# Kernel optimization log

Hardware: AMD Instinct MI355X
Metric: run time of the kernel (lower is better)

The kernel has to match this reference:

```python
import jax, jax.numpy as jnp
import numpy as np

NEG_SLOPE = 0.2


def _gat_layer(x, src, dst, W, att_src, att_dst, bias, concat):
    # x: [N, F_in]; W: [F_in, H*C]; att_*: [H, C]; bias: [H*C] or [C]
    N = x.shape[0]
    H, C = att_src.shape
    h = (x @ W).reshape(N, H, C)                      # [N, H, C]
    a_src = jnp.einsum('nhc,hc->nh', h, att_src)      # [N, H]
    a_dst = jnp.einsum('nhc,hc->nh', h, att_dst)      # [N, H]
    e = jax.nn.leaky_relu(a_src[src] + a_dst[dst], NEG_SLOPE)  # [E, H]
    # segment softmax over incoming edges of each destination node
    m = jax.ops.segment_max(e, dst, num_segments=N)   # [N, H]
    ex = jnp.exp(e - m[dst])
    s = jax.ops.segment_sum(ex, dst, num_segments=N)  # [N, H]
    alpha = ex / s[dst]                               # [E, H]
    out = jax.ops.segment_sum(h[src] * alpha[:, :, None], dst, num_segments=N)  # [N,H,C]
    out = out.reshape(N, H * C) if concat else out.mean(axis=1)
    return out + bias


def setup_inputs() -> dict:
    key = jax.random.key(0)
    ks = jax.random.split(key, 16)
    N, E, F = 50000, 1600000, 128
    HC1, H1 = 32, 4
    HC2, H2 = 32, 2
    NC, H3 = 2, 1     # layer3: 64 -> 2, 1 head, concat=False
    g = lambda k, shape, scale: jax.random.normal(k, shape, dtype=jnp.float32) * scale
    return {
        'x': g(ks[0], (N, F), 1.0),
        'edge_index': jax.random.randint(ks[1], (2, E), 0, N, dtype=jnp.int32),
        'W1': g(ks[2], (F, H1 * HC1), 0.1),
        'as1': g(ks[3], (H1, HC1), 0.1),
        'ad1': g(ks[4], (H1, HC1), 0.1),
        'b1': jnp.zeros((H1 * HC1,), jnp.float32),
        'W2': g(ks[5], (H1 * HC1, H2 * HC2), 0.1),
        'as2': g(ks[6], (H2, HC2), 0.1),
        'ad2': g(ks[7], (H2, HC2), 0.1),
        'b2': jnp.zeros((H2 * HC2,), jnp.float32),
        'W3': g(ks[8], (H2 * HC2, H3 * NC), 0.1),
        'as3': g(ks[9], (H3, NC), 0.1),
        'ad3': g(ks[10], (H3, NC), 0.1),
        'b3': jnp.zeros((NC,), jnp.float32),
    }


def reference(x, edge_index, W1, as1, ad1, b1, W2, as2, ad2, b2, W3, as3, ad3, b3):
    N = x.shape[0]
    # PyG GATConv adds self-loops by default
    loops = jnp.arange(N, dtype=edge_index.dtype)
    ei = jnp.concatenate([edge_index, jnp.stack([loops, loops])], axis=1)
    src, dst = ei[0], ei[1]
    h = _gat_layer(x, src, dst, W1, as1, ad1, b1, concat=True)
    h = jax.nn.elu(h)
    h = _gat_layer(h, src, dst, W2, as2, ad2, b2, concat=True)
    h = jax.nn.elu(h)
    h = _gat_layer(h, src, dst, W3, as3, ad3, b3, concat=False)
    return jax.nn.log_softmax(h, axis=1)
```

## Files before the change

### kernel.cpp

```cpp
#include <hip/hip_runtime.h>
#include <hip/hip_bf16.h>

#define NEG_SLOPE 0.2f
#define ARENA 10240

typedef __attribute__((ext_vector_type(8))) short short8v;
typedef __attribute__((ext_vector_type(4))) float f32x4;

__device__ __forceinline__ float bf_lo(uint32_t u) { return __uint_as_float(u << 16); }
__device__ __forceinline__ float bf_hi(uint32_t u) { return __uint_as_float(u & 0xffff0000u); }
__device__ __forceinline__ unsigned short f2bf(float f) {
    uint32_t u = __float_as_uint(f);
    u += 0x7fffu + ((u >> 16) & 1u);
    return (unsigned short)(u >> 16);
}
__device__ __forceinline__ float bf2f(unsigned short h) {
    return __uint_as_float((uint32_t)h << 16);
}

__device__ __forceinline__ int k_of(int l, int j) {
    return (l >> 4) * 4 + (j & 3) + 16 * (j >> 2);
}

template<int FIN, int FOUT>
__global__ void packW_kernel(const float* __restrict__ W, unsigned short* __restrict__ Wp) {
    constexpr int NT = FOUT / 16, KC = FIN / 32;
    int tid = blockIdx.x * blockDim.x + threadIdx.x;
    if (tid >= KC * NT * 64) return;
    int l  = tid & 63;
    int nt = (tid >> 6) % NT;
    int q  = tid / (64 * NT);
    int n  = nt * 16 + (l & 15);
    #pragma unroll
    for (int j = 0; j < 8; ++j) {
        int k = q * 32 + k_of(l, j);
        float v = W[k * FOUT + n];
        unsigned short h = f2bf(v);
        unsigned short lo = f2bf(v - bf2f(h));
        Wp[(((size_t)0 * KC + q) * NT + nt) * 512 + l * 8 + j] = h;
        Wp[(((size_t)1 * KC + q) * NT + nt) * 512 + l * 8 + j] = lo;
    }
}

template<int FIN, int FOUT, int H>
__global__ __launch_bounds__(256) void gemm_mfma_kernel(const float* __restrict__ X,
        const unsigned short* __restrict__ Wp, unsigned short* __restrict__ Hout,
        float* __restrict__ a_src, float* __restrict__ a_dst,
        const float* __restrict__ att_s, const float* __restrict__ att_d, int N) {
    constexpr int NT = FOUT / 16, KC = FIN / 32;
    __shared__ float sX[4][16 * FIN];
    int wv = threadIdx.x >> 6, l = threadIdx.x & 63;
    int mtile = blockIdx.x * 4 + wv;
    if (mtile * 16 >= N) return;
    const float* xsrc = X + (size_t)mtile * 16 * FIN;
    float* lds = sX[wv];
    #pragma unroll
    for (int i = 0; i < (16 * FIN) / 256; ++i) {
        int fi = (i * 64 + l) * 4;
        *(float4*)&lds[fi] = *(const float4*)&xsrc[fi];
    }
    __threadfence_block();

    int koff[8];
    #pragma unroll
    for (int j = 0; j < 8; ++j) koff[j] = k_of(l, j);
    int arow = (l & 15) * FIN;

    f32x4 acc[NT];
    #pragma unroll
    for (int nt = 0; nt < NT; ++nt) acc[nt] = f32x4{0.f, 0.f, 0.f, 0.f};

    const short8v* wp8 = (const short8v*)Wp;
    for (int q = 0; q < KC; ++q) {
        short8v ahi, alo;
        #pragma unroll
        for (int j = 0; j < 8; ++j) {
            float v = lds[arow + q * 32 + koff[j]];
            unsigned short h = f2bf(v);
            ahi[j] = (short)h;
            alo[j] = (short)f2bf(v - bf2f(h));
        }
        #pragma unroll
        for (int nt = 0; nt < NT; ++nt) {
            short8v bhi = wp8[((0 * KC + q) * NT + nt) * 64 + l];
            short8v blo = wp8[((1 * KC + q) * NT + nt) * 64 + l];
            acc[nt] = __builtin_amdgcn_mfma_f32_16x16x32_bf16(ahi, bhi, acc[nt], 0, 0, 0);
            acc[nt] = __builtin_amdgcn_mfma_f32_16x16x32_bf16(alo, bhi, acc[nt], 0, 0, 0);
            acc[nt] = __builtin_amdgcn_mfma_f32_16x16x32_bf16(ahi, blo, acc[nt], 0, 0, 0);
        }
    }

    float as_v[NT], ad_v[NT];
    #pragma unroll
    for (int nt = 0; nt < NT; ++nt) {
        as_v[nt] = att_s[nt * 16 + (l & 15)];
        ad_v[nt] = att_d[nt * 16 + (l & 15)];
    }
    float ps[4][H], pd[4][H];
    #pragma unroll
    for (int r = 0; r < 4; ++r)
        #pragma unroll
        for (int h = 0; h < H; ++h) { ps[r][h] = 0.f; pd[r][h] = 0.f; }
    #pragma unroll
    for (int nt = 0; nt < NT; ++nt)
        #pragma unroll
        for (int r = 0; r < 4; ++r) {
            ps[r][nt >> 1] += acc[nt][r] * as_v[nt];
            pd[r][nt >> 1] += acc[nt][r] * ad_v[nt];
        }
    constexpr int V = 4 * H;
    float* sc = lds;
    int g = l >> 4, l16 = l & 15;
    int base = g * 16 * V + l16 * V;
    __threadfence_block();
    #pragma unroll
    for (int r = 0; r < 4; ++r)
        #pragma unroll
        for (int h = 0; h < H; ++h) {
            sc[base + r * H + h]        = ps[r][h];
            sc[1024 + base + r * H + h] = pd[r][h];
        }
    __threadfence_block();
    if (l16 < V) {
        float S = 0.f, D = 0.f;
        #pragma unroll
        for (int x = 0; x < 16; ++x) {
            S += sc[g * 16 * V + x * V + l16];
            D += sc[1024 + g * 16 * V + x * V + l16];
        }
        int r = l16 / H, h = l16 % H;
        int row = mtile * 16 + g * 4 + r;
        a_src[row * H + h] = S;
        a_dst[row * H + h] = D;
    }

    int row0 = mtile * 16 + (l >> 4) * 4;
    int col  = l & 15;
    #pragma unroll
    for (int nt = 0; nt < NT; ++nt)
        #pragma unroll
        for (int r = 0; r < 4; ++r)
            Hout[(size_t)(row0 + r) * FOUT + nt * 16 + col] = f2bf(acc[nt][r]);
}

__global__ void arena_init_kernel(int* __restrict__ bcur) {
    bcur[threadIdx.x] = threadIdx.x * ARENA;
}

__global__ __launch_bounds__(256) void bkt_scatter_kernel(const int* __restrict__ src,
        const int* __restrict__ dst, int* __restrict__ bcur,
        uint32_t* __restrict__ packed, int E) {
    __shared__ int lh[256], lbase[256], lcur[256];
    int tid = threadIdx.x;
    lh[tid] = 0; lcur[tid] = 0;
    __syncthreads();
    int chunk = (E + gridDim.x - 1) / gridDim.x;
    int e0 = blockIdx.x * chunk;
    int e1 = min(E, e0 + chunk);
    for (int e = e0 + tid; e < e1; e += 256)
        atomicAdd(&lh[dst[e] >> 8], 1);
    __syncthreads();
    if (lh[tid]) lbase[tid] = atomicAdd(&bcur[tid], lh[tid]);
    __syncthreads();
    for (int e = e0 + tid; e < e1; e += 256) {
        int d = dst[e];
        int b = d >> 8;
        int pos = lbase[b] + atomicAdd(&lcur[b], 1);
        packed[pos] = ((uint32_t)(d & 255) << 16) | (uint32_t)src[e];
    }
}

__global__ __launch_bounds__(256) void bkt_sort_kernel(const uint32_t* __restrict__ packed,
        const int* __restrict__ bcur, int* __restrict__ row_ptr, int* __restrict__ degA,
        unsigned short* __restrict__ colw, int N) {
    __shared__ int lh[256], lexcl[256], lcur[256];
    __shared__ int ws4[4];
    int tid = threadIdx.x, lane = tid & 63, wid = tid >> 6;
    int B = blockIdx.x;
    int seg0 = B * ARENA, seg1 = bcur[B];
    lh[tid] = 0; lcur[tid] = 0;
    __syncthreads();
    for (int i = seg0 + tid; i < seg1; i += 256)
        atomicAdd(&lh[packed[i] >> 16], 1);
    __syncthreads();
    int v = lh[tid];
    int x = v;
    #pragma unroll
    for (int off = 1; off < 64; off <<= 1) {
        int t = __shfl_up(x, off);
        if (lane >= off) x += t;
    }
    if (lane == 63) ws4[wid] = x;
    __syncthreads();
    int add = 0;
    #pragma unroll
    for (int w = 0; w < 4; ++w) if (w < wid) add += ws4[w];
    int excl = add + x - v;
    lexcl[tid] = excl;
    int d = B * 256 + tid;
    if (d < N) { row_ptr[d] = seg0 + excl; degA[d] = v; }
    __syncthreads();
    for (int i = seg0 + tid; i < seg1; i += 256) {
        uint32_t p = packed[i];
        int bin = p >> 16;
        int pos = seg0 + lexcl[bin] + atomicAdd(&lcur[bin], 1);
        colw[pos] = (unsigned short)(p & 0xFFFF);
    }
}

template<int H, int C, bool ELU, bool FUSE3>
__global__ __launch_bounds__(256) void agg_fused_kernel(
        const unsigned short* __restrict__ Hb, const float* __restrict__ a_src,
        const float* __restrict__ a_dst, const int* __restrict__ row_ptr,
        const int* __restrict__ degA, const unsigned short* __restrict__ colw,
        const float* __restrict__ bias, float* __restrict__ out,
        const float* __restrict__ W3, const float* __restrict__ as3,
        const float* __restrict__ ad3, float* __restrict__ h3x4, int N) {
    constexpr int HC  = H * C;
    constexpr int LPW = HC / 8;
    constexpr int EPI = 64 / LPW;
    constexpr int SHIFT = (HC == 128) ? 8 : 7;
    static_assert(HC == 128 || HC == 64, "layout");
    __shared__ float sP[4][64 * H];
    __shared__ int   sS[4][64];
    int wv   = threadIdx.x >> 6;
    int lane = threadIdx.x & 63;
    int n = (int)(blockIdx.x * 4 + wv);
    if (n >= N) return;
    int start = row_ptr[n];
    int deg   = degA[n];

    float adv[H], cc[H], sp[H];
    #pragma unroll
    for (int h = 0; h < H; ++h) {
        adv[h] = a_dst[n * H + h];
        cc[h]  = fmaxf(adv[h], 0.f);
        sp[h]  = 0.f;
    }

    int sub = lane / LPW, pl = lane % LPW;
    int elem0 = pl * 8;
    int hh = elem0 / C;
    float a[8];
    #pragma unroll
    for (int j = 0; j < 8; ++j) a[j] = 0.f;

    for (int base = 0; base <= deg; base += 64) {
        int cnt = min(64, deg + 1 - base);
        int idx = base + lane;
        if (idx <= deg) {
            int srcn = (idx < deg) ? (int)colw[start + idx] : n;
            sS[wv][lane] = srcn;
            float av[H];
            if constexpr (H == 4) {
                float4 t = *(const float4*)&a_src[srcn * 4];
                av[0] = t.x; av[1] = t.y; av[2] = t.z; av[3] = t.w;
            } else {
                float2 t = *(const float2*)&a_src[srcn * 2];
                av[0] = t.x; av[1] = t.y;
            }
            #pragma unroll
            for (int h = 0; h < H; ++h) {
                float e = av[h] + adv[h];
                e = (e >= 0.f) ? e : NEG_SLOPE * e;
                float p = __expf(e - cc[h]);
                sp[h] += p;
                sP[wv][lane * H + h] = p;
            }
        }
        __threadfence_block();
        #pragma unroll 4
        for (int k = 0; k < cnt; k += EPI) {
            int eidx = k + sub;
            int eclm = min(eidx, cnt - 1);
            float w  = sP[wv][eclm * H + hh];
            int srcn = sS[wv][eclm];
            if (eidx >= cnt) w = 0.f;
            const char* pb = (const char*)Hb + (((size_t)srcn) << SHIFT) + elem0 * 2;
            uint4 pv = *(const uint4*)pb;
            a[0] = fmaf(w, bf_lo(pv.x), a[0]);
            a[1] = fmaf(w, bf_hi(pv.x), a[1]);
            a[2] = fmaf(w, bf_lo(pv.y), a[2]);
            a[3] = fmaf(w, bf_hi(pv.y), a[3]);
            a[4] = fmaf(w, bf_lo(pv.z), a[4]);
            a[5] = fmaf(w, bf_hi(pv.z), a[5]);
            a[6] = fmaf(w, bf_lo(pv.w), a[6]);
            a[7] = fmaf(w, bf_hi(pv.w), a[7]);
        }
        __threadfence_block();
    }

    #pragma unroll
    for (int off = 32; off; off >>= 1) {
        #pragma unroll
        for (int h = 0; h < H; ++h) sp[h] += __shfl_xor(sp[h], off);
    }
    #pragma unroll
    for (int off = 32; off >= LPW; off >>= 1) {
        #pragma unroll
        for (int j = 0; j < 8; ++j) a[j] += __shfl_xor(a[j], off);
    }
    float inv = 1.f / sp[hh];
    float v[8];
    float4 b40 = *(const float4*)&bias[elem0];
    float4 b41 = *(const float4*)&bias[elem0 + 4];
    v[0] = a[0] * inv + b40.x; v[1] = a[1] * inv + b40.y;
    v[2] = a[2] * inv + b40.z; v[3] = a[3] * inv + b40.w;
    v[4] = a[4] * inv + b41.x; v[5] = a[5] * inv + b41.y;
    v[6] = a[6] * inv + b41.z; v[7] = a[7] * inv + b41.w;
    if (ELU) {
        #pragma unroll
        for (int j = 0; j < 8; ++j) v[j] = (v[j] > 0.f) ? v[j] : __expf(v[j]) - 1.f;
    }
    if constexpr (!FUSE3) {
        if (sub == 0) {
            *(float4*)&out[(size_t)n * HC + elem0]     = make_float4(v[0], v[1], v[2], v[3]);
            *(float4*)&out[(size_t)n * HC + elem0 + 4] = make_float4(v[4], v[5], v[6], v[7]);
        }
    } else {
        float p0 = 0.f, p1 = 0.f;
        #pragma unroll
        for (int j = 0; j < 8; ++j) {
            p0 += v[j] * W3[(elem0 + j) * 2];
            p1 += v[j] * W3[(elem0 + j) * 2 + 1];
        }
        #pragma unroll
        for (int off = 4; off; off >>= 1) {
            p0 += __shfl_xor(p0, off);
            p1 += __shfl_xor(p1, off);
        }
        if (lane == 0) {
            float as = p0 * as3[0] + p1 * as3[1];
            float ad = p0 * ad3[0] + p1 * ad3[1];
            *(float4*)&h3x4[(size_t)n * 4] = make_float4(p0, p1, as, ad);
        }
    }
}

__global__ __launch_bounds__(256) void agg3_kernel(
        const float* __restrict__ h3x4, const int* __restrict__ row_ptr,
        const int* __restrict__ degA, const unsigned short* __restrict__ colw,
        const float* __restrict__ bias, float* __restrict__ out, int N) {
    int wave = (int)((blockIdx.x * blockDim.x + threadIdx.x) >> 6);
    int lane = threadIdx.x & 63;
    if (wave >= N) return;
    int n = wave;
    int start = row_ptr[n];
    int deg   = degA[n];
    float adv = h3x4[(size_t)n * 4 + 3];
    float c   = fmaxf(adv, 0.f);
    float s = 0.f, acc0 = 0.f, acc1 = 0.f;
    for (int i = lane; i <= deg; i += 64) {
        int srcn = (i < deg) ? (int)colw[start + i] : n;
        float4 g = *(const float4*)&h3x4[(size_t)srcn * 4];
        float e = g.z + adv;
        e = (e >= 0.f) ? e : NEG_SLOPE * e;
        float p = __expf(e - c);
        s += p;
        acc0 = fmaf(p, g.x, acc0);
        acc1 = fmaf(p, g.y, acc1);
    }
    #pragma unroll
    for (int off = 32; off; off >>= 1) {
        s    += __shfl_xor(s, off);
        acc0 += __shfl_xor(acc0, off);
        acc1 += __shfl_xor(acc1, off);
    }
    if (lane == 0) {
        float v0 = acc0 / s + bias[0];
        float v1 = acc1 / s + bias[1];
        float mx = fmaxf(v0, v1);
        float lse = mx + logf(__expf(v0 - mx) + __expf(v1 - mx));
        out[n * 2 + 0] = v0 - lse;
        out[n * 2 + 1] = v1 - lse;
    }
}

extern "C" void kernel_launch(void* const* d_in, const int* in_sizes, int n_in,
                              void* d_out, int out_size, void* d_ws, size_t ws_size,
                              hipStream_t stream) {
    const float* x   = (const float*)d_in[0];
    const int*   ei  = (const int*)d_in[1];
    const float* W1  = (const float*)d_in[2];
    const float* as1 = (const float*)d_in[3];
    const float* ad1 = (const float*)d_in[4];
    const float* b1  = (const float*)d_in[5];
    const float* W2  = (const float*)d_in[6];
    const float* as2 = (const float*)d_in[7];
    const float* ad2 = (const float*)d_in[8];
    const float* b2  = (const float*)d_in[9];
    const float* W3  = (const float*)d_in[10];
    const float* as3 = (const float*)d_in[11];
    const float* ad3 = (const float*)d_in[12];
    const float* b3  = (const float*)d_in[13];
    int N = in_sizes[0] / 128;
    int E = in_sizes[1] / 2;
    const int* src = ei;
    const int* dst = ei + E;
    int NB = (N + 255) / 256;

    char* ws = (char*)d_ws;
    size_t off = 0;
    auto alloc = [&](size_t bytes) -> void* {
        void* p = ws + off;
        off = (off + bytes + 255) & ~(size_t)255;
        return p;
    };
    int*            bcur    = (int*)alloc(256 * 4);
    int*            row_ptr = (int*)alloc((size_t)N * 4);
    int*            degA    = (int*)alloc((size_t)N * 4);
    uint32_t*       packed  = (uint32_t*)alloc((size_t)NB * ARENA * 4);
    unsigned short* colw    = (unsigned short*)alloc((size_t)NB * ARENA * 2);
    unsigned short* hb      = (unsigned short*)alloc((size_t)N * 128 * 2);
    float*          obuf    = (float*)alloc((size_t)N * 128 * 4);
    float*          h3x4    = (float*)alloc((size_t)N * 4 * 4);
    float*          asrc    = (float*)alloc((size_t)N * 4 * 4);
    float*          adst    = (float*)alloc((size_t)N * 4 * 4);
    unsigned short* Wp1     = (unsigned short*)alloc((size_t)2 * 4 * 8 * 512 * 2);
    unsigned short* Wp2     = (unsigned short*)alloc((size_t)2 * 4 * 4 * 512 * 2);

    packW_kernel<128, 128><<<8, 256, 0, stream>>>(W1, Wp1);
    packW_kernel<128, 64><<<4, 256, 0, stream>>>(W2, Wp2);

    arena_init_kernel<<<1, 256, 0, stream>>>(bcur);
    bkt_scatter_kernel<<<256, 256, 0, stream>>>(src, dst, bcur, packed, E);
    bkt_sort_kernel<<<NB, 256, 0, stream>>>(packed, bcur, row_ptr, degA, colw, N);

    int gmblocks = ((N + 15) / 16 + 3) / 4;

    gemm_mfma_kernel<128, 128, 4><<<gmblocks, 256, 0, stream>>>(x, Wp1, hb, asrc, adst, as1, ad1, N);
    agg_fused_kernel<4, 32, true, false><<<(N + 3) / 4, 256, 0, stream>>>(
        hb, asrc, adst, row_ptr, degA, colw, b1, obuf, nullptr, nullptr, nullptr, nullptr, N);

    gemm_mfma_kernel<128, 64, 2><<<gmblocks, 256, 0, stream>>>(obuf, Wp2, hb, asrc, adst, as2, ad2, N);
    agg_fused_kernel<2, 32, true, true><<<(N + 3) / 4, 256, 0, stream>>>(
        hb, asrc, adst, row_ptr, degA, colw, b2, nullptr, W3, as3, ad3, h3x4, N);

    agg3_kernel<<<(N + 3) / 4, 256, 0, stream>>>(h3x4, row_ptr, degA, colw, b3, (float*)d_out, N);
}
```

Baseline: 203.2 us.

## Store layer-1 output as bf16 and deepen gather pipelining in aggregation

Result: slower. 209.1 us (+2.9%).

```diff
diff --git a/kernel.cpp b/kernel.cpp
--- a/kernel.cpp
+++ b/kernel.cpp
@@ -90,6 +90,8 @@
         }
     }
 
+    constexpr int V = 4 * H;
+    constexpr int PLOFF = 64 * V;
     float as_v[NT], ad_v[NT];
     #pragma unroll
     for (int nt = 0; nt < NT; ++nt) {
@@ -108,7 +110,6 @@
             ps[r][nt >> 1] += acc[nt][r] * as_v[nt];
             pd[r][nt >> 1] += acc[nt][r] * ad_v[nt];
         }
-    constexpr int V = 4 * H;
     float* sc = lds;
     int g = l >> 4, l16 = l & 15;
     int base = g * 16 * V + l16 * V;
@@ -117,8 +118,8 @@
     for (int r = 0; r < 4; ++r)
         #pragma unroll
         for (int h = 0; h < H; ++h) {
-            sc[base + r * H + h]        = ps[r][h];
-            sc[1024 + base + r * H + h] = pd[r][h];
+            sc[base + r * H + h]         = ps[r][h];
+            sc[PLOFF + base + r * H + h] = pd[r][h];
         }
     __threadfence_block();
     if (l16 < V) {
@@ -126,7 +127,105 @@
         #pragma unroll
         for (int x = 0; x < 16; ++x) {
             S += sc[g * 16 * V + x * V + l16];
-            D += sc[1024 + g * 16 * V + x * V + l16];
+            D += sc[PLOFF + g * 16 * V + x * V + l16];
+        }
+        int r = l16 / H, h = l16 % H;
+        int row = mtile * 16 + g * 4 + r;
+        a_src[row * H + h] = S;
+        a_dst[row * H + h] = D;
+    }
+
+    int row0 = mtile * 16 + (l >> 4) * 4;
+    int col  = l & 15;
+    #pragma unroll
+    for (int nt = 0; nt < NT; ++nt)
+        #pragma unroll
+        for (int r = 0; r < 4; ++r)
+            Hout[(size_t)(row0 + r) * FOUT + nt * 16 + col] = f2bf(acc[nt][r]);
+}
+
+template<int FIN, int FOUT, int H>
+__global__ __launch_bounds__(256) void gemm_mfma_bf16_kernel(const unsigned short* __restrict__ X,
+        const unsigned short* __restrict__ Wp, unsigned short* __restrict__ Hout,
+        float* __restrict__ a_src, float* __restrict__ a_dst,
+        const float* __restrict__ att_s, const float* __restrict__ att_d, int N) {
+    constexpr int NT = FOUT / 16, KC = FIN / 32;
+    constexpr int V = 4 * H;
+    constexpr int PLOFF = 64 * V;
+    __shared__ float sX[4][(16 * FIN) / 2 > 2 * PLOFF ? (16 * FIN) / 2 : 2 * PLOFF];
+    int wv = threadIdx.x >> 6, l = threadIdx.x & 63;
+    int mtile = blockIdx.x * 4 + wv;
+    if (mtile * 16 >= N) return;
+    const unsigned short* xsrc = X + (size_t)mtile * 16 * FIN;
+    float* lds = sX[wv];
+    unsigned short* ldsu = (unsigned short*)lds;
+    #pragma unroll
+    for (int i = 0; i < (16 * FIN) / 512; ++i) {
+        int fi = (i * 64 + l) * 8;
+        *(uint4*)&ldsu[fi] = *(const uint4*)&xsrc[fi];
+    }
+    __threadfence_block();
+
+    int koff[8];
+    #pragma unroll
+    for (int j = 0; j < 8; ++j) koff[j] = k_of(l, j);
+    int arow = (l & 15) * FIN;
+
+    f32x4 acc[NT];
+    #pragma unroll
+    for (int nt = 0; nt < NT; ++nt) acc[nt] = f32x4{0.f, 0.f, 0.f, 0.f};
+
+    const short8v* wp8 = (const short8v*)Wp;
+    for (int q = 0; q < KC; ++q) {
+        short8v ahi;
+        #pragma unroll
+        for (int j = 0; j < 8; ++j)
+            ahi[j] = (short)ldsu[arow + q * 32 + koff[j]];
+        #pragma unroll
+        for (int nt = 0; nt < NT; ++nt) {
+            short8v bhi = wp8[((0 * KC + q) * NT + nt) * 64 + l];
+            short8v blo = wp8[((1 * KC + q) * NT + nt) * 64 + l];
+            acc[nt] = __builtin_amdgcn_mfma_f32_16x16x32_bf16(ahi, bhi, acc[nt], 0, 0, 0);
+            acc[nt] = __builtin_amdgcn_mfma_f32_16x16x32_bf16(ahi, blo, acc[nt], 0, 0, 0);
+        }
+    }
+
+    float as_v[NT], ad_v[NT];
+    #pragma unroll
+    for (int nt = 0; nt < NT; ++nt) {
+        as_v[nt] = att_s[nt * 16 + (l & 15)];
+        ad_v[nt] = att_d[nt * 16 + (l & 15)];
+    }
+    float ps[4][H], pd[4][H];
+    #pragma unroll
+    for (int r = 0; r < 4; ++r)
+        #pragma unroll
+        for (int h = 0; h < H; ++h) { ps[r][h] = 0.f; pd[r][h] = 0.f; }
+    #pragma unroll
+    for (int nt = 0; nt < NT; ++nt)
+        #pragma unroll
+        for (int r = 0; r < 4; ++r) {
+            ps[r][nt >> 1] += acc[nt][r] * as_v[nt];
+            pd[r][nt >> 1] += acc[nt][r] * ad_v[nt];
+        }
+    float* sc = lds;
+    int g = l >> 4, l16 = l & 15;
+    int base = g * 16 * V + l16 * V;
+    __threadfence_block();
+    #pragma unroll
+    for (int r = 0; r < 4; ++r)
+        #pragma unroll
+        for (int h = 0; h < H; ++h) {
+            sc[base + r * H + h]         = ps[r][h];
+            sc[PLOFF + base + r * H + h] = pd[r][h];
+        }
+    __threadfence_block();
+    if (l16 < V) {
+        float S = 0.f, D = 0.f;
+        #pragma unroll
+        for (int x = 0; x < 16; ++x) {
+            S += sc[g * 16 * V + x * V + l16];
+            D += sc[PLOFF + g * 16 * V + x * V + l16];
         }
         int r = l16 / H, h = l16 % H;
         int row = mtile * 16 + g * 4 + r;
@@ -213,16 +312,16 @@
         const unsigned short* __restrict__ Hb, const float* __restrict__ a_src,
         const float* __restrict__ a_dst, const int* __restrict__ row_ptr,
         const int* __restrict__ degA, const unsigned short* __restrict__ colw,
-        const float* __restrict__ bias, float* __restrict__ out,
+        const float* __restrict__ bias, unsigned short* __restrict__ outb,
         const float* __restrict__ W3, const float* __restrict__ as3,
         const float* __restrict__ ad3, float* __restrict__ h3x4, int N) {
     constexpr int HC  = H * C;
-    constexpr int LPW = HC / 8;
+    constexpr int LPW = HC / 4;
     constexpr int EPI = 64 / LPW;
+    constexpr int DEPTH = 8;
     constexpr int SHIFT = (HC == 128) ? 8 : 7;
     static_assert(HC == 128 || HC == 64, "layout");
-    __shared__ float sP[4][64 * H];
-    __shared__ int   sS[4][64];
+    __shared__ float2 sPS[4][64 * H];
     int wv   = threadIdx.x >> 6;
     int lane = threadIdx.x & 63;
     int n = (int)(blockIdx.x * 4 + wv);
@@ -239,18 +338,15 @@
     }
 
     int sub = lane / LPW, pl = lane % LPW;
-    int elem0 = pl * 8;
+    int elem0 = pl * 4;
     int hh = elem0 / C;
-    float a[8];
-    #pragma unroll
-    for (int j = 0; j < 8; ++j) a[j] = 0.f;
+    float a0 = 0.f, a1 = 0.f, a2 = 0.f, a3 = 0.f;
 
     for (int base = 0; base <= deg; base += 64) {
         int cnt = min(64, deg + 1 - base);
         int idx = base + lane;
         if (idx <= deg) {
             int srcn = (idx < deg) ? (int)colw[start + idx] : n;
-            sS[wv][lane] = srcn;
             float av[H];
             if constexpr (H == 4) {
                 float4 t = *(const float4*)&a_src[srcn * 4];
@@ -259,33 +355,38 @@
                 float2 t = *(const float2*)&a_src[srcn * 2];
                 av[0] = t.x; av[1] = t.y;
             }
+            float srcb = __int_as_float(srcn);
             #pragma unroll
             for (int h = 0; h < H; ++h) {
                 float e = av[h] + adv[h];
                 e = (e >= 0.f) ? e : NEG_SLOPE * e;
                 float p = __expf(e - cc[h]);
                 sp[h] += p;
-                sP[wv][lane * H + h] = p;
+                sPS[wv][lane * H + h] = make_float2(p, srcb);
             }
         }
         __threadfence_block();
-        #pragma unroll 4
-        for (int k = 0; k < cnt; k += EPI) {
-            int eidx = k + sub;
-            int eclm = min(eidx, cnt - 1);
-            float w  = sP[wv][eclm * H + hh];
-            int srcn = sS[wv][eclm];
-            if (eidx >= cnt) w = 0.f;
-            const char* pb = (const char*)Hb + (((size_t)srcn) << SHIFT) + elem0 * 2;
-            uint4 pv = *(const uint4*)pb;
-            a[0] = fmaf(w, bf_lo(pv.x), a[0]);
-            a[1] = fmaf(w, bf_hi(pv.x), a[1]);
-            a[2] = fmaf(w, bf_lo(pv.y), a[2]);
-            a[3] = fmaf(w, bf_hi(pv.y), a[3]);
-            a[4] = fmaf(w, bf_lo(pv.z), a[4]);
-            a[5] = fmaf(w, bf_hi(pv.z), a[5]);
-            a[6] = fmaf(w, bf_lo(pv.w), a[6]);
-            a[7] = fmaf(w, bf_hi(pv.w), a[7]);
+        for (int k = 0; k < cnt; k += EPI * DEPTH) {
+            float w[DEPTH]; int s[DEPTH];
+            #pragma unroll
+            for (int d = 0; d < DEPTH; ++d) {
+                int eidx = k + d * EPI + sub;
+                int eclm = min(eidx, cnt - 1);
+                float2 psv = sPS[wv][eclm * H + hh];
+                w[d] = (eidx < cnt) ? psv.x : 0.f;
+                s[d] = __float_as_int(psv.y);
+            }
+            uint2 pv[DEPTH];
+            #pragma unroll
+            for (int d = 0; d < DEPTH; ++d)
+                pv[d] = *(const uint2*)((const char*)Hb + (((size_t)s[d]) << SHIFT) + elem0 * 2);
+            #pragma unroll
+            for (int d = 0; d < DEPTH; ++d) {
+                a0 = fmaf(w[d], bf_lo(pv[d].x), a0);
+                a1 = fmaf(w[d], bf_hi(pv[d].x), a1);
+                a2 = fmaf(w[d], bf_lo(pv[d].y), a2);
+                a3 = fmaf(w[d], bf_hi(pv[d].y), a3);
+            }
         }
         __threadfence_block();
     }
@@ -297,35 +398,32 @@
     }
     #pragma unroll
     for (int off = 32; off >= LPW; off >>= 1) {
-        #pragma unroll
-        for (int j = 0; j < 8; ++j) a[j] += __shfl_xor(a[j], off);
+        a0 += __shfl_xor(a0, off); a1 += __shfl_xor(a1, off);
+        a2 += __shfl_xor(a2, off); a3 += __shfl_xor(a3, off);
     }
     float inv = 1.f / sp[hh];
-    float v[8];
-    float4 b40 = *(const float4*)&bias[elem0];
-    float4 b41 = *(const float4*)&bias[elem0 + 4];
-    v[0] = a[0] * inv + b40.x; v[1] = a[1] * inv + b40.y;
-    v[2] = a[2] * inv + b40.z; v[3] = a[3] * inv + b40.w;
-    v[4] = a[4] * inv + b41.x; v[5] = a[5] * inv + b41.y;
-    v[6] = a[6] * inv + b41.z; v[7] = a[7] * inv + b41.w;
+    float4 b4 = *(const float4*)&bias[elem0];
+    float v0 = a0 * inv + b4.x, v1 = a1 * inv + b4.y;
+    float v2 = a2 * inv + b4.z, v3 = a3 * inv + b4.w;
     if (ELU) {
-        #pragma unroll
-        for (int j = 0; j < 8; ++j) v[j] = (v[j] > 0.f) ? v[j] : __expf(v[j]) - 1.f;
+        v0 = (v0 > 0.f) ? v0 : __expf(v0) - 1.f;
+        v1 = (v1 > 0.f) ? v1 : __expf(v1) - 1.f;
+        v2 = (v2 > 0.f) ? v2 : __expf(v2) - 1.f;
+        v3 = (v3 > 0.f) ? v3 : __expf(v3) - 1.f;
     }
     if constexpr (!FUSE3) {
         if (sub == 0) {
-            *(float4*)&out[(size_t)n * HC + elem0]     = make_float4(v[0], v[1], v[2], v[3]);
-            *(float4*)&out[(size_t)n * HC + elem0 + 4] = make_float4(v[4], v[5], v[6], v[7]);
+            ushort4 o;
+            o.x = f2bf(v0); o.y = f2bf(v1); o.z = f2bf(v2); o.w = f2bf(v3);
+            *(ushort4*)&outb[(size_t)n * HC + elem0] = o;
         }
     } else {
-        float p0 = 0.f, p1 = 0.f;
-        #pragma unroll
-        for (int j = 0; j < 8; ++j) {
-            p0 += v[j] * W3[(elem0 + j) * 2];
-            p1 += v[j] * W3[(elem0 + j) * 2 + 1];
-        }
-        #pragma unroll
-        for (int off = 4; off; off >>= 1) {
+        float p0 = v0 * W3[elem0 * 2]     + v1 * W3[elem0 * 2 + 2]
+                 + v2 * W3[elem0 * 2 + 4] + v3 * W3[elem0 * 2 + 6];
+        float p1 = v0 * W3[elem0 * 2 + 1] + v1 * W3[elem0 * 2 + 3]
+                 + v2 * W3[elem0 * 2 + 5] + v3 * W3[elem0 * 2 + 7];
+        #pragma unroll
+        for (int off = 1; off < 16; off <<= 1) {
             p0 += __shfl_xor(p0, off);
             p1 += __shfl_xor(p1, off);
         }
@@ -412,7 +510,7 @@
     uint32_t*       packed  = (uint32_t*)alloc((size_t)NB * ARENA * 4);
     unsigned short* colw    = (unsigned short*)alloc((size_t)NB * ARENA * 2);
     unsigned short* hb      = (unsigned short*)alloc((size_t)N * 128 * 2);
-    float*          obuf    = (float*)alloc((size_t)N * 128 * 4);
+    unsigned short* obuf    = (unsigned short*)alloc((size_t)N * 128 * 2);
     float*          h3x4    = (float*)alloc((size_t)N * 4 * 4);
     float*          asrc    = (float*)alloc((size_t)N * 4 * 4);
     float*          adst    = (float*)alloc((size_t)N * 4 * 4);
@@ -432,7 +530,7 @@
     agg_fused_kernel<4, 32, true, false><<<(N + 3) / 4, 256, 0, stream>>>(
         hb, asrc, adst, row_ptr, degA, colw, b1, obuf, nullptr, nullptr, nullptr, nullptr, N);
 
-    gemm_mfma_kernel<128, 64, 2><<<gmblocks, 256, 0, stream>>>(obuf, Wp2, hb, asrc, adst, as2, ad2, N);
+    gemm_mfma_bf16_kernel<128, 64, 2><<<gmblocks, 256, 0, stream>>>(obuf, Wp2, hb, asrc, adst, as2, ad2, N);
     agg_fused_kernel<2, 32, true, true><<<(N + 3) / 4, 256, 0, stream>>>(
         hb, asrc, adst, row_ptr, degA, colw, b2, nullptr, W3, as3, ad3, h3x4, N);
 
```
